# Optimization experiments

Hardware: AMD Instinct MI355X
Metric: run time of the kernel (lower is better)

## Reference

```python
import jax, jax.numpy as jnp
import numpy as np

B, C, H, W = 1, 64, 512, 512
OUT_CH = 1
EPS = 1e-5


def conv2d(x, w, b, pad):
    y = jax.lax.conv_general_dilated(
        x, w, window_strides=(1, 1), padding=[(pad, pad), (pad, pad)],
        dimension_numbers=("NCHW", "OIHW", "NCHW"))
    return y + b[None, :, None, None]


def _bilinear_one(xb, py, px):
    # xb: [C,H,W]; py, px: [H,W] fractional sample coords; zero padding outside.
    Ch, Hh, Wh = xb.shape
    y0 = jnp.floor(py)
    x0 = jnp.floor(px)
    wy = py - y0
    wx = px - x0
    y0i = y0.astype(jnp.int32)
    x0i = x0.astype(jnp.int32)
    xf = xb.reshape(Ch, -1)

    def g(yi, xi):
        valid = (yi >= 0) & (yi < Hh) & (xi >= 0) & (xi < Wh)
        yc = jnp.clip(yi, 0, Hh - 1)
        xc = jnp.clip(xi, 0, Wh - 1)
        idx = (yc * Wh + xc).reshape(-1)
        v = xf[:, idx].reshape(Ch, Hh, Wh)
        return v * valid[None].astype(xb.dtype)

    v00 = g(y0i, x0i)
    v01 = g(y0i, x0i + 1)
    v10 = g(y0i + 1, x0i)
    v11 = g(y0i + 1, x0i + 1)
    return (v00 * (1 - wy) * (1 - wx) + v01 * (1 - wy) * wx
            + v10 * wy * (1 - wx) + v11 * wy * wx)


_bilinear = jax.vmap(_bilinear_one, in_axes=(0, 0, 0))


def deform_conv2d(x, offset, weight, bias):
    # torchvision DeformConv2d semantics: offset [B, 2*K, H, W], (dy, dx) per
    # kernel tap in row-major order, kernel 3x3, pad 1, stride 1.
    b, cin, h, w = x.shape
    off = offset.reshape(b, 9, 2, h, w)
    ii = jnp.arange(h, dtype=x.dtype)[:, None]  # [H,1]
    jj = jnp.arange(w, dtype=x.dtype)[None, :]  # [1,W]
    acc = jnp.zeros((b, weight.shape[0], h, w), dtype=x.dtype)
    for k in range(9):  # fixed small loop over kernel taps
        ky, kx = k // 3, k % 3
        py = ii + (ky - 1) + off[:, k, 0]  # [B,H,W]
        px = jj + (kx - 1) + off[:, k, 1]
        s = _bilinear(x, py, px)  # [B,Cin,H,W]
        acc = acc + jnp.einsum("bchw,oc->bohw", s, weight[:, :, ky, kx])
    return acc + bias[None, :, None, None]


def batchnorm(x, gamma, beta, mean, var):
    inv = gamma * jax.lax.rsqrt(var + EPS)
    return x * inv[None, :, None, None] + (beta - mean * inv)[None, :, None, None]


def setup_inputs() -> dict:
    key = jax.random.key(0)
    ks = jax.random.split(key, 16)
    d = {
        "x": jax.random.normal(ks[0], (B, C, H, W), jnp.float32),
        "offset1_w": jax.random.normal(ks[1], (18, C, 3, 3), jnp.float32) * 0.01,
        "offset1_b": jnp.zeros((18,), jnp.float32),
        "dcn1_w": jax.random.normal(ks[2], (C, C, 3, 3), jnp.float32) * 0.05,
        "dcn1_b": jnp.zeros((C,), jnp.float32),
        "bn1_gamma": jnp.ones((C,), jnp.float32),
        "bn1_beta": jnp.zeros((C,), jnp.float32),
        "bn1_mean": jax.random.normal(ks[3], (C,), jnp.float32) * 0.1,
        "bn1_var": jax.random.uniform(ks[4], (C,), jnp.float32, 0.5, 1.5),
        "offset2_w": jax.random.normal(ks[5], (18, C, 3, 3), jnp.float32) * 0.01,
        "offset2_b": jnp.zeros((18,), jnp.float32),
        "dcn2_w": jax.random.normal(ks[6], (C, C, 3, 3), jnp.float32) * 0.05,
        "dcn2_b": jnp.zeros((C,), jnp.float32),
        "bn2_gamma": jnp.ones((C,), jnp.float32),
        "bn2_beta": jnp.zeros((C,), jnp.float32),
        "bn2_mean": jax.random.normal(ks[7], (C,), jnp.float32) * 0.1,
        "bn2_var": jax.random.uniform(ks[8], (C,), jnp.float32, 0.5, 1.5),
        "conv_w": jax.random.normal(ks[9], (OUT_CH, C, 1, 1), jnp.float32) * 0.1,
        "conv_b": jnp.zeros((OUT_CH,), jnp.float32),
    }
    return d


def reference(x, offset1_w, offset1_b, dcn1_w, dcn1_b, bn1_gamma, bn1_beta,
              bn1_mean, bn1_var, offset2_w, offset2_b, dcn2_w, dcn2_b,
              bn2_gamma, bn2_beta, bn2_mean, bn2_var, conv_w, conv_b):
    off1 = conv2d(x, offset1_w, offset1_b, pad=1)
    h = deform_conv2d(x, off1, dcn1_w, dcn1_b)
    h = jax.nn.relu(batchnorm(h, bn1_gamma, bn1_beta, bn1_mean, bn1_var))
    off2 = conv2d(h, offset2_w, offset2_b, pad=1)
    h = deform_conv2d(h, off2, dcn2_w, dcn2_b)
    h = jax.nn.relu(batchnorm(h, bn2_gamma, bn2_beta, bn2_mean, bn2_var))
    return conv2d(h, conv_w, conv_b, pad=0)
```

## Files before the change

kernel.cpp:

```cpp
#include <hip/hip_runtime.h>
#include <math.h>

#define HWSZ (512*512)
#define EPSV 1e-5f

typedef _Float16 h8 __attribute__((ext_vector_type(8)));
typedef _Float16 h4 __attribute__((ext_vector_type(4)));
typedef _Float16 h2 __attribute__((ext_vector_type(2)));
typedef float    f32x4 __attribute__((ext_vector_type(4)));

__device__ __forceinline__ h8 as_h8(uint4 u) { return __builtin_bit_cast(h8, u); }
__device__ __forceinline__ uint4 as_u4(h8 v) { return __builtin_bit_cast(uint4, v); }

__device__ __forceinline__ int xcd_swz_4096(int bid) {
    return (bid & 7) * 512 + (bid >> 3);
}

__global__ __launch_bounds__(256) void to_hwc_f16(const float* __restrict__ in,
                                                  unsigned* __restrict__ out32) {
    __shared__ float T[64 * 65];
    int tid = threadIdx.x;
    int pbase = blockIdx.x * 64;
    int p = tid & 63, cg = tid >> 6;
#pragma unroll
    for (int j = 0; j < 16; ++j) {
        int c = cg * 16 + j;
        T[p * 65 + c] = in[c * HWSZ + pbase + p];
    }
    __syncthreads();
    int px = tid >> 2, cb = (tid & 3) * 16;
#pragma unroll
    for (int j = 0; j < 8; ++j) {
        int c = cb + 2 * j;
        h2 v = {(_Float16)T[px * 65 + c], (_Float16)T[px * 65 + c + 1]};
        out32[(pbase + px) * 32 + (c >> 1)] = __builtin_bit_cast(unsigned, v);
    }
}

__global__ __launch_bounds__(256) void prep_all(
        const float* __restrict__ dw1, const float* __restrict__ dw2,
        const float* __restrict__ ow1, const float* __restrict__ ow2,
        _Float16* __restrict__ wT1, _Float16* __restrict__ wT2,
        _Float16* __restrict__ wTo1, _Float16* __restrict__ wTo2) {
    int i = blockIdx.x * 256 + threadIdx.x;
    if (i < 36864) {
        int k = i / 4096, r = i % 4096;
        int s = r >> 9, o = (r >> 3) & 63, j = r & 7;
        int c = (s >> 2) * 32 + (s & 3) * 8 + j;
        wT1[i] = (_Float16)dw1[(o * 64 + c) * 9 + k];
    } else if (i < 73728) {
        int ii = i - 36864;
        int k = ii / 4096, r = ii % 4096;
        int s = r >> 9, o = (r >> 3) & 63, j = r & 7;
        int c = (s >> 2) * 32 + (s & 3) * 8 + j;
        wT2[ii] = (_Float16)dw2[(o * 64 + c) * 9 + k];
    } else if (i < 92160) {
        int j = i - 73728;
        int k = j / 2048, r = j % 2048, o = r >> 6, c = r & 63;
        wTo1[k * 2048 + o * 64 + c] = (_Float16)((o < 18) ? ow1[(o * 64 + c) * 9 + k] : 0.f);
    } else if (i < 110592) {
        int j = i - 92160;
        int k = j / 2048, r = j % 2048, o = r >> 6, c = r & 63;
        wTo2[k * 2048 + o * 64 + c] = (_Float16)((o < 18) ? ow2[(o * 64 + c) * 9 + k] : 0.f);
    }
}

__global__ __launch_bounds__(256, 4) void conv3x3_off_mfma(
        const _Float16* __restrict__ in, const _Float16* __restrict__ wTo,
        const float* __restrict__ bias, _Float16* __restrict__ off) {
    __shared__ uint4 TILE[3 * 66 * 8];

    int tid = threadIdx.x;
    int pbase = xcd_swz_4096(blockIdx.x) * 64;
    int y = pbase >> 9, xblk = pbase & 511;
    int l = tid & 63, wv = tid >> 6;
    int lq = l & 15, quad = l >> 4;
    int wn = wv & 1, wm = wv >> 1;

    h8 breg[18];
#pragma unroll
    for (int k = 0; k < 9; ++k)
#pragma unroll
        for (int kc = 0; kc < 2; ++kc)
            breg[k * 2 + kc] = *(const h8*)(wTo + k * 2048 + (wn * 16 + lq) * 64 + kc * 32 + quad * 8);

    uint4 v[7];
#pragma unroll
    for (int i = 0; i < 7; ++i) {
        int t = tid + 256 * i;
        int row = t / 528, r = t - row * 528;
        int col = r >> 3, cc = r & 7;
        int sy = y + row - 1, sx = xblk + col - 1;
        bool ok = (t < 1584) && ((unsigned)sy < 512u) && ((unsigned)sx < 512u);
        v[i] = ok ? *(const uint4*)(in + (sy * 512 + sx) * 64 + cc * 8)
                  : make_uint4(0u, 0u, 0u, 0u);
    }
#pragma unroll
    for (int i = 0; i < 7; ++i) {
        int t = tid + 256 * i;
        if (t < 1584) {
            int row = t / 528, r = t - row * 528;
            int col = r >> 3, cc = r & 7;
            TILE[(row * 66 + col) * 8 + (cc ^ (col & 7))] = v[i];
        }
    }
    __syncthreads();

    f32x4 zero = {0.f, 0.f, 0.f, 0.f};
    f32x4 acc[2]; acc[0] = zero; acc[1] = zero;

#pragma unroll
    for (int k = 0; k < 9; ++k) {
        int ky = k / 3, kx = k % 3;
#pragma unroll
        for (int kc = 0; kc < 2; ++kc) {
#pragma unroll
            for (int tm = 0; tm < 2; ++tm) {
                int col = kx + wm * 32 + tm * 16 + lq;
                int cc0 = kc * 4 + quad;
                h8 a = as_h8(TILE[(ky * 66 + col) * 8 + (cc0 ^ (col & 7))]);
                acc[tm] = __builtin_amdgcn_mfma_f32_16x16x32_f16(a, breg[k * 2 + kc], acc[tm], 0, 0, 0);
            }
        }
    }

    int n = wn * 16 + lq;
    if (n < 18) {
        float bb = bias[n];
#pragma unroll
        for (int tm = 0; tm < 2; ++tm)
#pragma unroll
            for (int reg = 0; reg < 4; ++reg) {
                int px = wm * 32 + tm * 16 + quad * 4 + reg;
                off[(pbase + px) * 18 + n] = (_Float16)(acc[tm][reg] + bb);
            }
    }
}

__global__ __launch_bounds__(256, 4) void dcn_fused(
        const _Float16* __restrict__ in, const _Float16* __restrict__ off,
        const _Float16* __restrict__ wTd, const float* __restrict__ bias,
        const float* __restrict__ gamma, const float* __restrict__ beta,
        const float* __restrict__ mean, const float* __restrict__ var,
        _Float16* __restrict__ out) {
    __shared__ uint4  WIN[196 * 8];
    __shared__ h4     SW9[9 * 64];
    __shared__ short4 SI9[9 * 64];
    __shared__ float  scl_s[64], sh_s[64];

    int tid = threadIdx.x;
    int bid = blockIdx.x;
    int ty = bid >> 6, tx = bid & 63;
    int r0 = ty * 8, c0 = tx * 8;
    int wr0 = r0 - 3, wc0 = c0 - 3;

    for (int t = tid; t < 576; t += 256) {
        int p = t & 63, k = t >> 6;
        int pr = p >> 3, pc = p & 7;
        int y = r0 + pr, x = c0 + pc;
        int gp = y * 512 + x;
        h2 dv = *(const h2*)(off + gp * 18 + 2 * k);
        float py = (float)(y + k / 3 - 1) + (float)dv[0];
        float px = (float)(x + k % 3 - 1) + (float)dv[1];
        float y0f = floorf(py), x0f = floorf(px);
        float wy = py - y0f, wx = px - x0f;
        int y0 = (int)y0f, x0 = (int)x0f;
        int y1 = y0 + 1, x1 = x0 + 1;
        float vy0 = ((unsigned)y0 < 512u) ? 1.f : 0.f;
        float vy1 = ((unsigned)y1 < 512u) ? 1.f : 0.f;
        float vx0 = ((unsigned)x0 < 512u) ? 1.f : 0.f;
        float vx1 = ((unsigned)x1 < 512u) ? 1.f : 0.f;
        SW9[t] = (h4){(_Float16)((1.f - wy) * (1.f - wx) * vy0 * vx0),
                      (_Float16)((1.f - wy) * wx * vy0 * vx1),
                      (_Float16)(wy * (1.f - wx) * vy1 * vx0),
                      (_Float16)(wy * wx * vy1 * vx1)};
        int y0c = min(max(y0, 0), 511), y1c = min(max(y1, 0), 511);
        int x0c = min(max(x0, 0), 511), x1c = min(max(x1, 0), 511);
        SI9[t] = make_short4((short)(y0c - wr0), (short)(x0c - wc0),
                             (short)(y1c - wr0), (short)(x1c - wc0));
    }
    if (tid < 64) {
        float s = gamma[tid] * rsqrtf(var[tid] + EPSV);
        scl_s[tid] = s;
        sh_s[tid] = beta[tid] - mean[tid] * s + bias[tid] * s;
    }

    uint4 sv[7];
#pragma unroll
    for (int i = 0; i < 7; ++i) {
        int t = tid + 256 * i;
        int wp = t >> 3, cc = t & 7;
        int wi = wp / 14, wj = wp - wi * 14;
        int sy = wr0 + wi, sx = wc0 + wj;
        bool ok = (t < 1568) && ((unsigned)sy < 512u) && ((unsigned)sx < 512u);
        sv[i] = ok ? *(const uint4*)(in + ((sy << 9) + sx) * 64 + cc * 8)
                   : make_uint4(0u, 0u, 0u, 0u);
    }
#pragma unroll
    for (int i = 0; i < 7; ++i) {
        int t = tid + 256 * i;
        if (t < 1568) {
            int wp = t >> 3, cc = t & 7;
            WIN[wp * 8 + (cc ^ (wp & 7))] = sv[i];
        }
    }
    __syncthreads();

    int l = tid & 63, wv = tid >> 6;
    int lq = l & 15, quad = l >> 4;
    int pxl = wv * 16 + lq;

#define CORNER(LO, HI, WY, WX) do {                                           \
        int wy_ = (WY), wx_ = (WX);                                           \
        if ((unsigned)wy_ < 14u && (unsigned)wx_ < 14u) {                     \
            int wp_ = wy_ * 14 + wx_;                                         \
            int sw_ = wp_ & 7;                                                \
            LO = as_h8(WIN[wp_ * 8 + (quad ^ sw_)]);                          \
            HI = as_h8(WIN[wp_ * 8 + ((quad + 4) ^ sw_)]);                    \
        } else {                                                              \
            int iy_ = wy_ + wr0, ix_ = wx_ + wc0;                             \
            const _Float16* g_ = in + ((iy_ << 9) + ix_) * 64 + quad * 8;     \
            LO = *(const h8*)g_;                                              \
            HI = *(const h8*)(g_ + 32);                                       \
        }                                                                     \
    } while (0)

    f32x4 zero = {0.f, 0.f, 0.f, 0.f};
    f32x4 acc[4];
    acc[0] = zero; acc[1] = zero; acc[2] = zero; acc[3] = zero;

#pragma unroll
    for (int k = 0; k < 9; ++k) {
        const _Float16* wk = wTd + k * 4096;
        h8 bl[4], bh[4];
#pragma unroll
        for (int nb = 0; nb < 4; ++nb) {
            bl[nb] = *(const h8*)(wk + (quad * 64 + nb * 16 + lq) * 8);
            bh[nb] = *(const h8*)(wk + ((quad + 4) * 64 + nb * 16 + lq) * 8);
        }
        short4 s = SI9[k * 64 + pxl];
        h4 w = SW9[k * 64 + pxl];
        h8 c0l, c0h, c1l, c1h, c2l, c2h, c3l, c3h;
        CORNER(c0l, c0h, (int)s.x, (int)s.y);
        CORNER(c1l, c1h, (int)s.x, (int)s.w);
        CORNER(c2l, c2h, (int)s.z, (int)s.y);
        CORNER(c3l, c3h, (int)s.z, (int)s.w);
        h8 alo = c0l * w[0] + c1l * w[1] + c2l * w[2] + c3l * w[3];
        h8 ahi = c0h * w[0] + c1h * w[1] + c2h * w[2] + c3h * w[3];
#pragma unroll
        for (int nb = 0; nb < 4; ++nb)
            acc[nb] = __builtin_amdgcn_mfma_f32_16x16x32_f16(alo, bl[nb], acc[nb], 0, 0, 0);
#pragma unroll
        for (int nb = 0; nb < 4; ++nb)
            acc[nb] = __builtin_amdgcn_mfma_f32_16x16x32_f16(ahi, bh[nb], acc[nb], 0, 0, 0);
    }
#undef CORNER

#pragma unroll
    for (int nb = 0; nb < 4; ++nb) {
        float sc = scl_s[nb * 16 + lq];
        float sh = sh_s[nb * 16 + lq];
#pragma unroll
        for (int reg = 0; reg < 4; ++reg) {
            int p_out = wv * 16 + quad * 4 + reg;
            int gp = (r0 + (p_out >> 3)) * 512 + c0 + (p_out & 7);
            out[gp * 64 + nb * 16 + lq] =
                (_Float16)fmaxf(fmaf(acc[nb][reg], sc, sh), 0.f);
        }
    }
}

__global__ __launch_bounds__(256) void conv1x1_out(const _Float16* __restrict__ in,
                                                   const float* __restrict__ w,
                                                   const float* __restrict__ b,
                                                   float* __restrict__ out) {
    int p = blockIdx.x * 256 + threadIdx.x;
    float acc = b[0];
    const h8* ip = (const h8*)(in + p * 64);
#pragma unroll
    for (int j = 0; j < 8; ++j) {
        h8 v = ip[j];
#pragma unroll
        for (int e = 0; e < 8; ++e)
            acc = fmaf((float)v[e], w[j * 8 + e], acc);
    }
    out[p] = acc;
}

extern "C" void kernel_launch(void* const* d_in, const int* in_sizes, int n_in,
                              void* d_out, int out_size, void* d_ws, size_t ws_size,
                              hipStream_t stream) {
    const float* x      = (const float*)d_in[0];
    const float* off1_w = (const float*)d_in[1];
    const float* off1_b = (const float*)d_in[2];
    const float* dcn1_w = (const float*)d_in[3];
    const float* dcn1_b = (const float*)d_in[4];
    const float* bn1_g  = (const float*)d_in[5];
    const float* bn1_be = (const float*)d_in[6];
    const float* bn1_m  = (const float*)d_in[7];
    const float* bn1_v  = (const float*)d_in[8];
    const float* off2_w = (const float*)d_in[9];
    const float* off2_b = (const float*)d_in[10];
    const float* dcn2_w = (const float*)d_in[11];
    const float* dcn2_b = (const float*)d_in[12];
    const float* bn2_g  = (const float*)d_in[13];
    const float* bn2_be = (const float*)d_in[14];
    const float* bn2_m  = (const float*)d_in[15];
    const float* bn2_v  = (const float*)d_in[16];
    const float* conv_w = (const float*)d_in[17];
    const float* conv_b = (const float*)d_in[18];
    float* out = (float*)d_out;

    char* ws = (char*)d_ws;
    _Float16* xh   = (_Float16*)ws;
    _Float16* h1   = (_Float16*)(ws + 33554432);
    _Float16* offb = (_Float16*)(ws + 2 * 33554432);
    _Float16* wT1  = (_Float16*)(ws + 2 * 33554432 + 9437184);
    _Float16* wT2  = wT1 + 36864;
    _Float16* wTo1 = wT2 + 36864;
    _Float16* wTo2 = wTo1 + 18432;
    _Float16* h2 = xh;

    prep_all<<<432, 256, 0, stream>>>(dcn1_w, dcn2_w, off1_w, off2_w,
                                      wT1, wT2, wTo1, wTo2);
    to_hwc_f16<<<4096, 256, 0, stream>>>(x, (unsigned*)xh);

    conv3x3_off_mfma<<<4096, 256, 0, stream>>>(xh, wTo1, off1_b, offb);
    dcn_fused<<<4096, 256, 0, stream>>>(xh, offb, wT1, dcn1_b,
                                        bn1_g, bn1_be, bn1_m, bn1_v, h1);
    conv3x3_off_mfma<<<4096, 256, 0, stream>>>(h1, wTo2, off2_b, offb);
    dcn_fused<<<4096, 256, 0, stream>>>(h1, offb, wT2, dcn2_b,
                                        bn2_g, bn2_be, bn2_m, bn2_v, h2);
    conv1x1_out<<<1024, 256, 0, stream>>>(h2, conv_w, conv_b, out);
}
```

Before: 320.3 us.

## Fuse offset 3x3 conv into deformable conv kernel using shared window tile

Removes the separate offset-convolution kernel and computes the 18 offset channels inside dcn_fused with MFMA, reading from the 14x14 input window already staged in LDS. The offsets go to a small LDS buffer instead of a global workspace. This drops two kernel launches and the global write and read of the offset tensor, as well as the duplicate halo loads. In exchange, each DCN block does extra MFMA work, loads offset weights from global per wave, and adds one more barrier, which may raise register pressure.

```diff
diff --git a/kernel.cpp b/kernel.cpp
--- a/kernel.cpp
+++ b/kernel.cpp
@@ -11,10 +11,6 @@
 
 __device__ __forceinline__ h8 as_h8(uint4 u) { return __builtin_bit_cast(h8, u); }
 __device__ __forceinline__ uint4 as_u4(h8 v) { return __builtin_bit_cast(uint4, v); }
-
-__device__ __forceinline__ int xcd_swz_4096(int bid) {
-    return (bid & 7) * 512 + (bid >> 3);
-}
 
 __global__ __launch_bounds__(256) void to_hwc_f16(const float* __restrict__ in,
                                                   unsigned* __restrict__ out32) {
@@ -65,88 +61,18 @@
     }
 }
 
-__global__ __launch_bounds__(256, 4) void conv3x3_off_mfma(
+__global__ __launch_bounds__(256, 4) void dcn_fused(
         const _Float16* __restrict__ in, const _Float16* __restrict__ wTo,
-        const float* __restrict__ bias, _Float16* __restrict__ off) {
-    __shared__ uint4 TILE[3 * 66 * 8];
-
-    int tid = threadIdx.x;
-    int pbase = xcd_swz_4096(blockIdx.x) * 64;
-    int y = pbase >> 9, xblk = pbase & 511;
-    int l = tid & 63, wv = tid >> 6;
-    int lq = l & 15, quad = l >> 4;
-    int wn = wv & 1, wm = wv >> 1;
-
-    h8 breg[18];
-#pragma unroll
-    for (int k = 0; k < 9; ++k)
-#pragma unroll
-        for (int kc = 0; kc < 2; ++kc)
-            breg[k * 2 + kc] = *(const h8*)(wTo + k * 2048 + (wn * 16 + lq) * 64 + kc * 32 + quad * 8);
-
-    uint4 v[7];
-#pragma unroll
-    for (int i = 0; i < 7; ++i) {
-        int t = tid + 256 * i;
-        int row = t / 528, r = t - row * 528;
-        int col = r >> 3, cc = r & 7;
-        int sy = y + row - 1, sx = xblk + col - 1;
-        bool ok = (t < 1584) && ((unsigned)sy < 512u) && ((unsigned)sx < 512u);
-        v[i] = ok ? *(const uint4*)(in + (sy * 512 + sx) * 64 + cc * 8)
-                  : make_uint4(0u, 0u, 0u, 0u);
-    }
-#pragma unroll
-    for (int i = 0; i < 7; ++i) {
-        int t = tid + 256 * i;
-        if (t < 1584) {
-            int row = t / 528, r = t - row * 528;
-            int col = r >> 3, cc = r & 7;
-            TILE[(row * 66 + col) * 8 + (cc ^ (col & 7))] = v[i];
-        }
-    }
-    __syncthreads();
-
-    f32x4 zero = {0.f, 0.f, 0.f, 0.f};
-    f32x4 acc[2]; acc[0] = zero; acc[1] = zero;
-
-#pragma unroll
-    for (int k = 0; k < 9; ++k) {
-        int ky = k / 3, kx = k % 3;
-#pragma unroll
-        for (int kc = 0; kc < 2; ++kc) {
-#pragma unroll
-            for (int tm = 0; tm < 2; ++tm) {
-                int col = kx + wm * 32 + tm * 16 + lq;
-                int cc0 = kc * 4 + quad;
-                h8 a = as_h8(TILE[(ky * 66 + col) * 8 + (cc0 ^ (col & 7))]);
-                acc[tm] = __builtin_amdgcn_mfma_f32_16x16x32_f16(a, breg[k * 2 + kc], acc[tm], 0, 0, 0);
-            }
-        }
-    }
-
-    int n = wn * 16 + lq;
-    if (n < 18) {
-        float bb = bias[n];
-#pragma unroll
-        for (int tm = 0; tm < 2; ++tm)
-#pragma unroll
-            for (int reg = 0; reg < 4; ++reg) {
-                int px = wm * 32 + tm * 16 + quad * 4 + reg;
-                off[(pbase + px) * 18 + n] = (_Float16)(acc[tm][reg] + bb);
-            }
-    }
-}
-
-__global__ __launch_bounds__(256, 4) void dcn_fused(
-        const _Float16* __restrict__ in, const _Float16* __restrict__ off,
+        const float* __restrict__ off_bias,
         const _Float16* __restrict__ wTd, const float* __restrict__ bias,
         const float* __restrict__ gamma, const float* __restrict__ beta,
         const float* __restrict__ mean, const float* __restrict__ var,
         _Float16* __restrict__ out) {
-    __shared__ uint4  WIN[196 * 8];
-    __shared__ h4     SW9[9 * 64];
-    __shared__ short4 SI9[9 * 64];
-    __shared__ float  scl_s[64], sh_s[64];
+    __shared__ uint4    WIN[196 * 8];
+    __shared__ h4       SW9[9 * 64];
+    __shared__ short4   SI9[9 * 64];
+    __shared__ _Float16 OFFB[64][20];
+    __shared__ float    scl_s[64], sh_s[64];
 
     int tid = threadIdx.x;
     int bid = blockIdx.x;
@@ -154,12 +80,75 @@
     int r0 = ty * 8, c0 = tx * 8;
     int wr0 = r0 - 3, wc0 = c0 - 3;
 
+    if (tid < 64) {
+        float s = gamma[tid] * rsqrtf(var[tid] + EPSV);
+        scl_s[tid] = s;
+        sh_s[tid] = beta[tid] - mean[tid] * s + bias[tid] * s;
+    }
+
+    uint4 sv[7];
+#pragma unroll
+    for (int i = 0; i < 7; ++i) {
+        int t = tid + 256 * i;
+        int wp = t >> 3, cc = t & 7;
+        int wi = wp / 14, wj = wp - wi * 14;
+        int sy = wr0 + wi, sx = wc0 + wj;
+        bool ok = (t < 1568) && ((unsigned)sy < 512u) && ((unsigned)sx < 512u);
+        sv[i] = ok ? *(const uint4*)(in + ((sy << 9) + sx) * 64 + cc * 8)
+                   : make_uint4(0u, 0u, 0u, 0u);
+    }
+#pragma unroll
+    for (int i = 0; i < 7; ++i) {
+        int t = tid + 256 * i;
+        if (t < 1568) {
+            int wp = t >> 3, cc = t & 7;
+            WIN[wp * 8 + (cc ^ (wp & 7))] = sv[i];
+        }
+    }
+    __syncthreads();
+
+    int l = tid & 63, wv = tid >> 6;
+    int lq = l & 15, quad = l >> 4;
+    int pxl = wv * 16 + lq;
+
+    {
+        int pr = pxl >> 3, pc = pxl & 7;
+        int wpb = (pr + 3) * 14 + (pc + 3);
+        f32x4 zero = {0.f, 0.f, 0.f, 0.f};
+        f32x4 oacc[2]; oacc[0] = zero; oacc[1] = zero;
+#pragma unroll
+        for (int k = 0; k < 9; ++k) {
+            int wp = wpb + (k / 3 - 1) * 14 + (k % 3 - 1);
+            int sw = wp & 7;
+            h8 alo = as_h8(WIN[wp * 8 + (quad ^ sw)]);
+            h8 ahi = as_h8(WIN[wp * 8 + ((quad + 4) ^ sw)]);
+            const _Float16* wk = wTo + k * 2048;
+#pragma unroll
+            for (int h = 0; h < 2; ++h) {
+                h8 b0 = *(const h8*)(wk + (h * 16 + lq) * 64 + quad * 8);
+                h8 b1 = *(const h8*)(wk + (h * 16 + lq) * 64 + 32 + quad * 8);
+                oacc[h] = __builtin_amdgcn_mfma_f32_16x16x32_f16(alo, b0, oacc[h], 0, 0, 0);
+                oacc[h] = __builtin_amdgcn_mfma_f32_16x16x32_f16(ahi, b1, oacc[h], 0, 0, 0);
+            }
+        }
+#pragma unroll
+        for (int h = 0; h < 2; ++h) {
+            int oc = h * 16 + lq;
+            if (oc < 18) {
+                float bb = off_bias[oc];
+#pragma unroll
+                for (int reg = 0; reg < 4; ++reg)
+                    OFFB[wv * 16 + quad * 4 + reg][oc] = (_Float16)(oacc[h][reg] + bb);
+            }
+        }
+    }
+    __syncthreads();
+
     for (int t = tid; t < 576; t += 256) {
         int p = t & 63, k = t >> 6;
         int pr = p >> 3, pc = p & 7;
         int y = r0 + pr, x = c0 + pc;
-        int gp = y * 512 + x;
-        h2 dv = *(const h2*)(off + gp * 18 + 2 * k);
+        h2 dv = *(const h2*)&OFFB[p][2 * k];
         float py = (float)(y + k / 3 - 1) + (float)dv[0];
         float px = (float)(x + k % 3 - 1) + (float)dv[1];
         float y0f = floorf(py), x0f = floorf(px);
@@ -179,36 +168,7 @@
         SI9[t] = make_short4((short)(y0c - wr0), (short)(x0c - wc0),
                              (short)(y1c - wr0), (short)(x1c - wc0));
     }
-    if (tid < 64) {
-        float s = gamma[tid] * rsqrtf(var[tid] + EPSV);
-        scl_s[tid] = s;
-        sh_s[tid] = beta[tid] - mean[tid] * s + bias[tid] * s;
-    }
-
-    uint4 sv[7];
-#pragma unroll
-    for (int i = 0; i < 7; ++i) {
-        int t = tid + 256 * i;
-        int wp = t >> 3, cc = t & 7;
-        int wi = wp / 14, wj = wp - wi * 14;
-        int sy = wr0 + wi, sx = wc0 + wj;
-        bool ok = (t < 1568) && ((unsigned)sy < 512u) && ((unsigned)sx < 512u);
-        sv[i] = ok ? *(const uint4*)(in + ((sy << 9) + sx) * 64 + cc * 8)
-                   : make_uint4(0u, 0u, 0u, 0u);
-    }
-#pragma unroll
-    for (int i = 0; i < 7; ++i) {
-        int t = tid + 256 * i;
-        if (t < 1568) {
-            int wp = t >> 3, cc = t & 7;
-            WIN[wp * 8 + (cc ^ (wp & 7))] = sv[i];
-        }
-    }
-    __syncthreads();
-
-    int l = tid & 63, wv = tid >> 6;
-    int lq = l & 15, quad = l >> 4;
-    int pxl = wv * 16 + lq;
+    __syncthreads();
 
 #define CORNER(LO, HI, WY, WX) do {                                           \
         int wy_ = (WY), wx_ = (WX);                                           \
@@ -314,8 +274,7 @@
     char* ws = (char*)d_ws;
     _Float16* xh   = (_Float16*)ws;
     _Float16* h1   = (_Float16*)(ws + 33554432);
-    _Float16* offb = (_Float16*)(ws + 2 * 33554432);
-    _Float16* wT1  = (_Float16*)(ws + 2 * 33554432 + 9437184);
+    _Float16* wT1  = (_Float16*)(ws + 2 * 33554432);
     _Float16* wT2  = wT1 + 36864;
     _Float16* wTo1 = wT2 + 36864;
     _Float16* wTo2 = wTo1 + 18432;
@@ -325,11 +284,9 @@
                                       wT1, wT2, wTo1, wTo2);
     to_hwc_f16<<<4096, 256, 0, stream>>>(x, (unsigned*)xh);
 
-    conv3x3_off_mfma<<<4096, 256, 0, stream>>>(xh, wTo1, off1_b, offb);
-    dcn_fused<<<4096, 256, 0, stream>>>(xh, offb, wT1, dcn1_b,
+    dcn_fused<<<4096, 256, 0, stream>>>(xh, wTo1, off1_b, wT1, dcn1_b,
                                         bn1_g, bn1_be, bn1_m, bn1_v, h1);
-    conv3x3_off_mfma<<<4096, 256, 0, stream>>>(h1, wTo2, off2_b, offb);
-    dcn_fused<<<4096, 256, 0, stream>>>(h1, offb, wT2, dcn2_b,
+    dcn_fused<<<4096, 256, 0, stream>>>(h1, wTo2, off2_b, wT2, dcn2_b,
                                         bn2_g, bn2_be, bn2_m, bn2_v, h2);
     conv1x1_out<<<1024, 256, 0, stream>>>(h2, conv_w, conv_b, out);
 }
```

Result: slower. 355.6 us (+11.0%).
